# Performance work log

Hardware: AMD Instinct MI355X
Metric: run time of the kernel (lower is better)

The kernel has to match this reference:

```python
import jax, jax.numpy as jnp
import numpy as np

B, S, IN_DIM, H, NC = 4, 512, 32, 64, 3

def setup_inputs() -> dict:
    key = jax.random.key(0)
    ks = jax.random.split(key, 20)
    def lin(k, i, o):
        bound = 1.0 / np.sqrt(i)
        kw, kb = jax.random.split(k)
        W = jax.random.uniform(kw, (i, o), jnp.float32, -bound, bound)
        b = jax.random.uniform(kb, (o,), jnp.float32, -bound, bound)
        return W, b
    W1, b1 = lin(ks[0], IN_DIM, H)
    W2, b2 = lin(ks[1], H, H)
    We1, be1 = lin(ks[2], 2 * H, H)
    We2, be2 = lin(ks[3], H, H)
    Wd1, bd1 = lin(ks[4], 2 * H, H // 2)
    Wd2, bd2 = lin(ks[5], H // 2, 1)
    Wc1, bc1 = lin(ks[6], 2 * H, 32)
    Wc2, bc2 = lin(ks[7], 32, NC)
    x = jax.random.normal(ks[8], (B, S, IN_DIM), jnp.float32)
    return {"x": x, "W1": W1, "b1": b1, "W2": W2, "b2": b2,
            "We1": We1, "be1": be1, "We2": We2, "be2": be2,
            "Wd1": Wd1, "bd1": bd1, "Wd2": Wd2, "bd2": bd2,
            "Wc1": Wc1, "bc1": bc1, "Wc2": Wc2, "bc2": bc2}

def reference(x, W1, b1, W2, b2, We1, be1, We2, be2,
              Wd1, bd1, Wd2, bd2, Wc1, bc1, Wc2, bc2):
    b, s, _ = x.shape
    # node encoder: Linear -> ReLU -> Linear
    nodes = jax.nn.relu(x @ W1 + b1) @ W2 + b2          # [b,s,H]
    h = nodes.shape[-1]
    # all-pairs concat: pairs[b,i,j] = [nodes[b,i], nodes[b,j]]
    pi = jnp.broadcast_to(nodes[:, :, None, :], (b, s, s, h))
    pj = jnp.broadcast_to(nodes[:, None, :, :], (b, s, s, h))
    pairs = jnp.concatenate([pi, pj], axis=-1)          # [b,s,s,2H]
    # edge network
    raw_msgs = jax.nn.relu(pairs @ We1 + be1) @ We2 + be2   # [b,s,s,H]
    # demon gate
    keep = jax.nn.sigmoid(jax.nn.relu(pairs @ Wd1 + bd1) @ Wd2 + bd2)  # [b,s,s,1]
    active = (raw_msgs * keep).sum(axis=2)              # [b,s,H]
    trash = (raw_msgs * (1.0 - keep)).sum(axis=2)       # [b,s,H]
    main_emb = (nodes + active).mean(axis=1)            # [b,H]
    trash_emb = trash.mean(axis=1)                      # [b,H]
    feat = jnp.concatenate([main_emb, trash_emb], axis=-1)  # [b,2H]
    return jax.nn.relu(feat @ Wc1 + bc1) @ Wc2 + bc2    # [b,NC]
```

## Files before the change

kernel.cpp:

```cpp
#include <hip/hip_runtime.h>

#define BB 4
#define SS 512
#define IND 32
#define HH 64
#define NCC 3

#define IPB 4
#define NPB (BB * 256)
#define NNB 512

#define OFF_U    0
#define OFF_V    (OFF_U + BB*SS*HH)
#define OFF_P    (OFF_V + BB*SS*HH)
#define OFF_QT   (OFF_P + BB*SS*32)
#define OFF_SN   (OFF_QT + 32*BB*SS)
#define OFF_SA   (OFF_SN + NNB*HH)
#define OFF_SH   (OFF_SA + NPB*HH)
#define OFF_SKP  (OFF_SH + NPB*HH)

__device__ __forceinline__ float rl(float v, int l) {
    return __uint_as_float(__builtin_amdgcn_readlane(__float_as_uint(v), l));
}

__global__ __launch_bounds__(256) void k_nodes(
    const float* __restrict__ x,  const float* __restrict__ W1, const float* __restrict__ b1,
    const float* __restrict__ W2, const float* __restrict__ b2,
    const float* __restrict__ We1,const float* __restrict__ be1,
    const float* __restrict__ Wd1,const float* __restrict__ bd1,
    float* __restrict__ ws)
{
    float* U = ws + OFF_U;  float* V4 = ws + OFF_V;
    float* P = ws + OFF_P;  float* Qt4 = ws + OFF_QT;
    float* SN = ws + OFF_SN;
    __shared__ float sn_lds[4][64];
    const int tid = threadIdx.x, wave = tid >> 6, lane = tid & 63;
    const int node = blockIdx.x * 4 + wave;

    float xv = (lane < IND) ? x[node * IND + lane] : 0.0f;
    float h1 = b1[lane];
    #pragma unroll
    for (int k = 0; k < IND; k++)
        h1 = fmaf(__shfl(xv, k, 64), W1[k * HH + lane], h1);
    h1 = fmaxf(h1, 0.0f);

    float nd = b2[lane];
    #pragma unroll 16
    for (int k = 0; k < HH; k++)
        nd = fmaf(__shfl(h1, k, 64), W2[k * HH + lane], nd);

    float uv = be1[lane];
    float vv = 0.0f;
    float pq = (lane < 32) ? bd1[lane] : 0.0f;
    const float* WdCol = (lane < 32) ? (Wd1 + lane) : (Wd1 + HH * 32 + (lane - 32));
    #pragma unroll 16
    for (int k = 0; k < HH; k++) {
        float s = __shfl(nd, k, 64);
        uv = fmaf(s, We1[k * HH + lane], uv);
        vv = fmaf(s, We1[(HH + k) * HH + lane], vv);
        pq = fmaf(s, WdCol[k * 32], pq);
    }
    U[node * HH + lane] = uv;
    V4[(blockIdx.x * 64 + lane) * 4 + wave] = vv;
    if (lane < 32) {
        P[node * 32 + lane] = pq;
    } else {
        int k = lane - 32;
        Qt4[((k >> 2) * (BB * SS) + node) * 4 + (k & 3)] = pq;
    }

    sn_lds[wave][lane] = nd;
    __syncthreads();
    if (tid < 64)
        SN[blockIdx.x * 64 + tid] = (sn_lds[0][tid] + sn_lds[1][tid]) + (sn_lds[2][tid] + sn_lds[3][tid]);
}

__global__ __launch_bounds__(256, 4) void k_pairs(
    const float* __restrict__ wd2, const float* __restrict__ bd2,
    float* __restrict__ ws)
{
    const float*  U   = ws + OFF_U;
    const float4* V4  = (const float4*)(ws + OFF_V);
    const float*  P   = ws + OFF_P;
    const float4* Qt4 = (const float4*)(ws + OFF_QT);
    float* SA = ws + OFF_SA;  float* SHo = ws + OFF_SH;  float* SKp = ws + OFF_SKP;

    __shared__ float4 gs[4][64];
    __shared__ float redA[4][64], redH[4][64], redK[4];

    const int tid = threadIdx.x, wave = tid >> 6, lane = tid & 63;
    const int b  = blockIdx.x >> 8;
    const int ic = (blockIdx.x >> 1) & 127;
    const int jc = blockIdx.x & 1;
    const int i0 = ic * IPB;
    const int jbase = b * SS + jc * 256 + wave * 64;

    const float4* Qp = Qt4 + jbase + lane;
    const float4* Vp = V4 + (jbase >> 2) * 64 + lane;
    float4 q[8], v[16];
    #pragma unroll
    for (int kg = 0; kg < 8; kg++) q[kg] = Qp[kg * (BB * SS)];
    #pragma unroll
    for (int jq = 0; jq < 8; jq++) v[jq] = Vp[jq * 64];

    const float u0 = U[(b * SS + i0 + 0) * HH + lane];
    const float u1 = U[(b * SS + i0 + 1) * HH + lane];
    const float u2 = U[(b * SS + i0 + 2) * HH + lane];
    const float u3 = U[(b * SS + i0 + 3) * HH + lane];
    const float pk0 = P[(b * SS + i0 + 0) * 32 + (lane & 31)];
    const float pk1 = P[(b * SS + i0 + 1) * 32 + (lane & 31)];
    const float pk2 = P[(b * SS + i0 + 2) * 32 + (lane & 31)];
    const float pk3 = P[(b * SS + i0 + 3) * 32 + (lane & 31)];
    const float wv  = wd2[lane & 31];
    const float bd2v = bd2[0];

    float a0 = bd2v, a1 = bd2v, a2 = bd2v, a3 = bd2v;
    #pragma unroll
    for (int kg = 0; kg < 8; kg++) {
        #pragma unroll
        for (int t = 0; t < 4; t++) {
            const int k = kg * 4 + t;
            float qv = (t == 0) ? q[kg].x : (t == 1) ? q[kg].y : (t == 2) ? q[kg].z : q[kg].w;
            float w  = rl(wv, k);
            a0 = fmaf(w, fmaxf(rl(pk0, k) + qv, 0.0f), a0);
            a1 = fmaf(w, fmaxf(rl(pk1, k) + qv, 0.0f), a1);
            a2 = fmaf(w, fmaxf(rl(pk2, k) + qv, 0.0f), a2);
            a3 = fmaf(w, fmaxf(rl(pk3, k) + qv, 0.0f), a3);
        }
    }
    float g0 = 1.0f / (1.0f + __expf(-a0));
    float g1 = 1.0f / (1.0f + __expf(-a1));
    float g2 = 1.0f / (1.0f + __expf(-a2));
    float g3 = 1.0f / (1.0f + __expf(-a3));
    float sk = (g0 + g1) + (g2 + g3);
    gs[wave][lane] = make_float4(g0, g1, g2, g3);

    #pragma unroll
    for (int jq = 8; jq < 16; jq++) v[jq] = Vp[jq * 64];
    __builtin_amdgcn_wave_barrier();

    float sa = 0.0f, sh = 0.0f;
    #pragma unroll
    for (int jq = 0; jq < 16; jq++) {
        #pragma unroll
        for (int t = 0; t < 4; t++) {
            float vv = (t == 0) ? v[jq].x : (t == 1) ? v[jq].y : (t == 2) ? v[jq].z : v[jq].w;
            float4 g4 = gs[wave][jq * 4 + t];
            float h0 = fmaxf(u0 + vv, 0.0f);
            float h1 = fmaxf(u1 + vv, 0.0f);
            float h2 = fmaxf(u2 + vv, 0.0f);
            float h3 = fmaxf(u3 + vv, 0.0f);
            sh += (h0 + h1) + (h2 + h3);
            sa = fmaf(g4.x, h0, sa);
            sa = fmaf(g4.y, h1, sa);
            sa = fmaf(g4.z, h2, sa);
            sa = fmaf(g4.w, h3, sa);
        }
    }

    redA[wave][lane] = sa;
    redH[wave][lane] = sh;
    #pragma unroll
    for (int off = 32; off; off >>= 1) sk += __shfl_xor(sk, off, 64);
    if (lane == 0) redK[wave] = sk;
    __syncthreads();

    if (tid < 64) {
        SA[blockIdx.x * 64 + tid]  = (redA[0][tid] + redA[1][tid]) + (redA[2][tid] + redA[3][tid]);
        SHo[blockIdx.x * 64 + tid] = (redH[0][tid] + redH[1][tid]) + (redH[2][tid] + redH[3][tid]);
        if (tid == 0)
            SKp[blockIdx.x * 16] = (redK[0] + redK[1]) + (redK[2] + redK[3]);
    }
}

__global__ __launch_bounds__(256) void k_final(
    const float* __restrict__ We2, const float* __restrict__ be2,
    const float* __restrict__ Wc1, const float* __restrict__ bc1,
    const float* __restrict__ Wc2, const float* __restrict__ bc2,
    const float* __restrict__ ws, float* __restrict__ out)
{
    const float4* SN4 = (const float4*)(ws + OFF_SN);
    const float4* SA4 = (const float4*)(ws + OFF_SA);
    const float4* SH4 = (const float4*)(ws + OFF_SH);
    const float*  SKp = ws + OFF_SKP;
    __shared__ float4 r4[3][16][16];
    __shared__ float redS[256], saL[64], shL[64];
    __shared__ float featL[128], c1L[32];
    const int tid = threadIdx.x, wave = tid >> 6, lane = tid & 63;
    const int grp = tid >> 4, l16 = tid & 15;
    const int b = blockIdx.x;

    float4 sn4 = make_float4(0.f, 0.f, 0.f, 0.f);
    float4 sa4 = sn4, sh4 = sn4;
    #pragma unroll
    for (int r = 0; r < 8; r++) {
        float4 t = SN4[(b * 128 + r * 16 + grp) * 16 + l16];
        sn4.x += t.x; sn4.y += t.y; sn4.z += t.z; sn4.w += t.w;
    }
    #pragma unroll
    for (int r = 0; r < 16; r++) {
        float4 t = SA4[(b * 256 + r * 16 + grp) * 16 + l16];
        float4 u = SH4[(b * 256 + r * 16 + grp) * 16 + l16];
        sa4.x += t.x; sa4.y += t.y; sa4.z += t.z; sa4.w += t.w;
        sh4.x += u.x; sh4.y += u.y; sh4.z += u.z; sh4.w += u.w;
    }
    r4[0][grp][l16] = sn4;  r4[1][grp][l16] = sa4;  r4[2][grp][l16] = sh4;
    redS[tid] = SKp[(b * 256 + tid) * 16];
    __syncthreads();

    if (wave == 0) {
        const int li = lane >> 2, comp = lane & 3;
        float snT = 0.f, saF = 0.f, shF = 0.f;
        #pragma unroll
        for (int g = 0; g < 16; g++) {
            snT += ((const float*)&r4[0][g][li])[comp];
            saF += ((const float*)&r4[1][g][li])[comp];
            shF += ((const float*)&r4[2][g][li])[comp];
        }
        float skp = (redS[lane] + redS[64 + lane]) + (redS[128 + lane] + redS[192 + lane]);
        #pragma unroll
        for (int off = 32; off; off >>= 1) skp += __shfl_xor(skp, off, 64);
        saL[lane] = saF;  shL[lane] = shF;

        float as = skp * be2[lane];
        float ts = (262144.0f - skp) * be2[lane];
        #pragma unroll 8
        for (int k = 0; k < HH; k++) {
            float w = We2[k * HH + lane];
            float sak = saL[k];
            as = fmaf(sak, w, as);
            ts = fmaf(shL[k] - sak, w, ts);
        }
        featL[lane]      = (snT + as) * (1.0f / 512.0f);
        featL[64 + lane] = ts * (1.0f / 512.0f);
    }
    __syncthreads();

    if (tid < 32) {
        float c1 = bc1[tid];
        #pragma unroll 8
        for (int k = 0; k < 128; k++)
            c1 = fmaf(featL[k], Wc1[k * 32 + tid], c1);
        c1L[tid] = fmaxf(c1, 0.0f);
    }
    __syncthreads();
    if (tid < NCC) {
        float o = bc2[tid];
        #pragma unroll
        for (int k = 0; k < 32; k++)
            o = fmaf(c1L[k], Wc2[k * NCC + tid], o);
        out[b * NCC + tid] = o;
    }
}

extern "C" void kernel_launch(void* const* d_in, const int* in_sizes, int n_in,
                              void* d_out, int out_size, void* d_ws, size_t ws_size,
                              hipStream_t stream) {
    const float* x   = (const float*)d_in[0];
    const float* W1  = (const float*)d_in[1];
    const float* b1  = (const float*)d_in[2];
    const float* W2  = (const float*)d_in[3];
    const float* b2  = (const float*)d_in[4];
    const float* We1 = (const float*)d_in[5];
    const float* be1 = (const float*)d_in[6];
    const float* We2 = (const float*)d_in[7];
    const float* be2 = (const float*)d_in[8];
    const float* Wd1 = (const float*)d_in[9];
    const float* bd1 = (const float*)d_in[10];
    const float* wd2 = (const float*)d_in[11];
    const float* bd2 = (const float*)d_in[12];
    const float* Wc1 = (const float*)d_in[13];
    const float* bc1 = (const float*)d_in[14];
    const float* Wc2 = (const float*)d_in[15];
    const float* bc2 = (const float*)d_in[16];
    float* ws  = (float*)d_ws;
    float* out = (float*)d_out;

    k_nodes<<<dim3(NNB), dim3(256), 0, stream>>>(x, W1, b1, W2, b2, We1, be1, Wd1, bd1, ws);
    k_pairs<<<dim3(NPB), dim3(256), 0, stream>>>(wd2, bd2, ws);
    k_final<<<dim3(BB), dim3(256), 0, stream>>>(We2, be2, Wc1, bc1, Wc2, bc2, ws, out);
}
```

Before: 34.07 us.

## Process eight query nodes per pair block and read gate weights from memory

Measured after the change: 34.09 us. About the same (+0.1%).

```diff
diff --git a/kernel.cpp b/kernel.cpp
--- a/kernel.cpp
+++ b/kernel.cpp
@@ -6,8 +6,8 @@
 #define HH 64
 #define NCC 3
 
-#define IPB 4
-#define NPB (BB * 256)
+#define IPB 8
+#define NPB (BB * 128)
 #define NNB 512
 
 #define OFF_U    0
@@ -18,10 +18,6 @@
 #define OFF_SA   (OFF_SN + NNB*HH)
 #define OFF_SH   (OFF_SA + NPB*HH)
 #define OFF_SKP  (OFF_SH + NPB*HH)
-
-__device__ __forceinline__ float rl(float v, int l) {
-    return __uint_as_float(__builtin_amdgcn_readlane(__float_as_uint(v), l));
-}
 
 __global__ __launch_bounds__(256) void k_nodes(
     const float* __restrict__ x,  const float* __restrict__ W1, const float* __restrict__ b1,
@@ -75,7 +71,7 @@
         SN[blockIdx.x * 64 + tid] = (sn_lds[0][tid] + sn_lds[1][tid]) + (sn_lds[2][tid] + sn_lds[3][tid]);
 }
 
-__global__ __launch_bounds__(256, 4) void k_pairs(
+__global__ __launch_bounds__(256, 2) void k_pairs(
     const float* __restrict__ wd2, const float* __restrict__ bd2,
     float* __restrict__ ws)
 {
@@ -85,12 +81,12 @@
     const float4* Qt4 = (const float4*)(ws + OFF_QT);
     float* SA = ws + OFF_SA;  float* SHo = ws + OFF_SH;  float* SKp = ws + OFF_SKP;
 
-    __shared__ float4 gs[4][64];
+    __shared__ float4 gsA[4][64], gsB[4][64];
     __shared__ float redA[4][64], redH[4][64], redK[4];
 
     const int tid = threadIdx.x, wave = tid >> 6, lane = tid & 63;
-    const int b  = blockIdx.x >> 8;
-    const int ic = (blockIdx.x >> 1) & 127;
+    const int b  = blockIdx.x >> 7;
+    const int ic = (blockIdx.x >> 1) & 63;
     const int jc = blockIdx.x & 1;
     const int i0 = ic * IPB;
     const int jbase = b * SS + jc * 256 + wave * 64;
@@ -101,64 +97,71 @@
     #pragma unroll
     for (int kg = 0; kg < 8; kg++) q[kg] = Qp[kg * (BB * SS)];
     #pragma unroll
-    for (int jq = 0; jq < 8; jq++) v[jq] = Vp[jq * 64];
-
-    const float u0 = U[(b * SS + i0 + 0) * HH + lane];
-    const float u1 = U[(b * SS + i0 + 1) * HH + lane];
-    const float u2 = U[(b * SS + i0 + 2) * HH + lane];
-    const float u3 = U[(b * SS + i0 + 3) * HH + lane];
-    const float pk0 = P[(b * SS + i0 + 0) * 32 + (lane & 31)];
-    const float pk1 = P[(b * SS + i0 + 1) * 32 + (lane & 31)];
-    const float pk2 = P[(b * SS + i0 + 2) * 32 + (lane & 31)];
-    const float pk3 = P[(b * SS + i0 + 3) * 32 + (lane & 31)];
-    const float wv  = wd2[lane & 31];
+    for (int jq = 0; jq < 16; jq++) v[jq] = Vp[jq * 64];
+
+    float u[IPB];
+    #pragma unroll
+    for (int i = 0; i < IPB; i++) u[i] = U[(b * SS + i0 + i) * HH + lane];
+
+    const float* Pb = P + (b * SS + i0) * 32;
     const float bd2v = bd2[0];
 
-    float a0 = bd2v, a1 = bd2v, a2 = bd2v, a3 = bd2v;
+    float a[IPB];
+    #pragma unroll
+    for (int i = 0; i < IPB; i++) a[i] = bd2v;
     #pragma unroll
     for (int kg = 0; kg < 8; kg++) {
         #pragma unroll
         for (int t = 0; t < 4; t++) {
             const int k = kg * 4 + t;
             float qv = (t == 0) ? q[kg].x : (t == 1) ? q[kg].y : (t == 2) ? q[kg].z : q[kg].w;
-            float w  = rl(wv, k);
-            a0 = fmaf(w, fmaxf(rl(pk0, k) + qv, 0.0f), a0);
-            a1 = fmaf(w, fmaxf(rl(pk1, k) + qv, 0.0f), a1);
-            a2 = fmaf(w, fmaxf(rl(pk2, k) + qv, 0.0f), a2);
-            a3 = fmaf(w, fmaxf(rl(pk3, k) + qv, 0.0f), a3);
-        }
-    }
-    float g0 = 1.0f / (1.0f + __expf(-a0));
-    float g1 = 1.0f / (1.0f + __expf(-a1));
-    float g2 = 1.0f / (1.0f + __expf(-a2));
-    float g3 = 1.0f / (1.0f + __expf(-a3));
-    float sk = (g0 + g1) + (g2 + g3);
-    gs[wave][lane] = make_float4(g0, g1, g2, g3);
-
-    #pragma unroll
-    for (int jq = 8; jq < 16; jq++) v[jq] = Vp[jq * 64];
+            float w  = wd2[k];
+            #pragma unroll
+            for (int i = 0; i < IPB; i++)
+                a[i] = fmaf(w, fmaxf(Pb[i * 32 + k] + qv, 0.0f), a[i]);
+        }
+    }
+    float g[IPB], sk = 0.0f;
+    #pragma unroll
+    for (int i = 0; i < IPB; i++) {
+        g[i] = 1.0f / (1.0f + __expf(-a[i]));
+        sk += g[i];
+    }
+    gsA[wave][lane] = make_float4(g[0], g[1], g[2], g[3]);
+    gsB[wave][lane] = make_float4(g[4], g[5], g[6], g[7]);
     __builtin_amdgcn_wave_barrier();
 
-    float sa = 0.0f, sh = 0.0f;
+    float sa[IPB] = {0,0,0,0,0,0,0,0};
+    float sh = 0.0f;
     #pragma unroll
     for (int jq = 0; jq < 16; jq++) {
         #pragma unroll
         for (int t = 0; t < 4; t++) {
             float vv = (t == 0) ? v[jq].x : (t == 1) ? v[jq].y : (t == 2) ? v[jq].z : v[jq].w;
-            float4 g4 = gs[wave][jq * 4 + t];
-            float h0 = fmaxf(u0 + vv, 0.0f);
-            float h1 = fmaxf(u1 + vv, 0.0f);
-            float h2 = fmaxf(u2 + vv, 0.0f);
-            float h3 = fmaxf(u3 + vv, 0.0f);
-            sh += (h0 + h1) + (h2 + h3);
-            sa = fmaf(g4.x, h0, sa);
-            sa = fmaf(g4.y, h1, sa);
-            sa = fmaf(g4.z, h2, sa);
-            sa = fmaf(g4.w, h3, sa);
-        }
-    }
-
-    redA[wave][lane] = sa;
+            float4 ga = gsA[wave][jq * 4 + t];
+            float4 gb = gsB[wave][jq * 4 + t];
+            float h0 = fmaxf(u[0] + vv, 0.0f);
+            float h1 = fmaxf(u[1] + vv, 0.0f);
+            float h2 = fmaxf(u[2] + vv, 0.0f);
+            float h3 = fmaxf(u[3] + vv, 0.0f);
+            float h4 = fmaxf(u[4] + vv, 0.0f);
+            float h5 = fmaxf(u[5] + vv, 0.0f);
+            float h6 = fmaxf(u[6] + vv, 0.0f);
+            float h7 = fmaxf(u[7] + vv, 0.0f);
+            sh += ((h0 + h1) + (h2 + h3)) + ((h4 + h5) + (h6 + h7));
+            sa[0] = fmaf(ga.x, h0, sa[0]);
+            sa[1] = fmaf(ga.y, h1, sa[1]);
+            sa[2] = fmaf(ga.z, h2, sa[2]);
+            sa[3] = fmaf(ga.w, h3, sa[3]);
+            sa[4] = fmaf(gb.x, h4, sa[4]);
+            sa[5] = fmaf(gb.y, h5, sa[5]);
+            sa[6] = fmaf(gb.z, h6, sa[6]);
+            sa[7] = fmaf(gb.w, h7, sa[7]);
+        }
+    }
+    float saT = ((sa[0] + sa[1]) + (sa[2] + sa[3])) + ((sa[4] + sa[5]) + (sa[6] + sa[7]));
+
+    redA[wave][lane] = saT;
     redH[wave][lane] = sh;
     #pragma unroll
     for (int off = 32; off; off >>= 1) sk += __shfl_xor(sk, off, 64);
@@ -184,7 +187,7 @@
     const float4* SH4 = (const float4*)(ws + OFF_SH);
     const float*  SKp = ws + OFF_SKP;
     __shared__ float4 r4[3][16][16];
-    __shared__ float redS[256], saL[64], shL[64];
+    __shared__ float redS[128], saL[64], shL[64];
     __shared__ float featL[128], c1L[32];
     const int tid = threadIdx.x, wave = tid >> 6, lane = tid & 63;
     const int grp = tid >> 4, l16 = tid & 15;
@@ -194,18 +197,15 @@
     float4 sa4 = sn4, sh4 = sn4;
     #pragma unroll
     for (int r = 0; r < 8; r++) {
-        float4 t = SN4[(b * 128 + r * 16 + grp) * 16 + l16];
-        sn4.x += t.x; sn4.y += t.y; sn4.z += t.z; sn4.w += t.w;
-    }
-    #pragma unroll
-    for (int r = 0; r < 16; r++) {
-        float4 t = SA4[(b * 256 + r * 16 + grp) * 16 + l16];
-        float4 u = SH4[(b * 256 + r * 16 + grp) * 16 + l16];
-        sa4.x += t.x; sa4.y += t.y; sa4.z += t.z; sa4.w += t.w;
-        sh4.x += u.x; sh4.y += u.y; sh4.z += u.z; sh4.w += u.w;
+        float4 t0 = SN4[(b * 128 + r * 16 + grp) * 16 + l16];
+        float4 t1 = SA4[(b * 128 + r * 16 + grp) * 16 + l16];
+        float4 t2 = SH4[(b * 128 + r * 16 + grp) * 16 + l16];
+        sn4.x += t0.x; sn4.y += t0.y; sn4.z += t0.z; sn4.w += t0.w;
+        sa4.x += t1.x; sa4.y += t1.y; sa4.z += t1.z; sa4.w += t1.w;
+        sh4.x += t2.x; sh4.y += t2.y; sh4.z += t2.z; sh4.w += t2.w;
     }
     r4[0][grp][l16] = sn4;  r4[1][grp][l16] = sa4;  r4[2][grp][l16] = sh4;
-    redS[tid] = SKp[(b * 256 + tid) * 16];
+    if (tid < 128) redS[tid] = SKp[(b * 128 + tid) * 16];
     __syncthreads();
 
     if (wave == 0) {
@@ -217,7 +217,7 @@
             saF += ((const float*)&r4[1][g][li])[comp];
             shF += ((const float*)&r4[2][g][li])[comp];
         }
-        float skp = (redS[lane] + redS[64 + lane]) + (redS[128 + lane] + redS[192 + lane]);
+        float skp = redS[lane] + redS[64 + lane];
         #pragma unroll
         for (int off = 32; off; off >>= 1) skp += __shfl_xor(skp, off, 64);
         saL[lane] = saF;  shL[lane] = shF;
```
